# Kernel optimization log

Hardware: AMD Instinct MI355X
Metric: run time of the kernel (lower is better)

Reference implementation:

```python
import jax, jax.numpy as jnp
import numpy as np

B, N, D = 32, 512, 1024
H, DH = 8, 64
INNER = H * DH          # 512
PROJ = 512
MID = (D + PROJ) // 2   # 768
EPS = 1e-5


def _ln(x, gamma):
    # F.layer_norm over last dim, beta is a zeros buffer
    m = jnp.mean(x, axis=-1, keepdims=True)
    v = jnp.var(x, axis=-1, keepdims=True)
    return (x - m) * jax.lax.rsqrt(v + EPS) * gamma


def setup_inputs() -> dict:
    key = jax.random.key(0)
    ks = jax.random.split(key, 12)
    s = 0.02
    return {
        "x": jax.random.normal(ks[0], (B, N, D), dtype=jnp.float32),
        "pos_encoding": jax.random.normal(ks[1], (1, N, D), dtype=jnp.float32),
        "queries": jax.random.normal(ks[2], (N, D), dtype=jnp.float32),
        "ln_q_g": jnp.ones((D,), dtype=jnp.float32),
        "ln_ctx_g": jnp.ones((D,), dtype=jnp.float32),
        "Wq": jax.random.normal(ks[3], (D, INNER), dtype=jnp.float32) * s,
        "Wkv": jax.random.normal(ks[4], (D, 2 * DH), dtype=jnp.float32) * s,
        "Wout": jax.random.normal(ks[5], (INNER, D), dtype=jnp.float32) * s,
        "ln_post_g": jnp.ones((D,), dtype=jnp.float32),
        "W1": jax.random.normal(ks[6], (D, MID), dtype=jnp.float32) * s,
        "b1": jnp.zeros((MID,), dtype=jnp.float32),
        "W2": jax.random.normal(ks[7], (MID, PROJ), dtype=jnp.float32) * s,
        "b2": jnp.zeros((PROJ,), dtype=jnp.float32),
        "zero_masks": jnp.ones((B, N), dtype=jnp.int32),  # unused (masking commented out in source)
    }


def reference(x, pos_encoding, queries, ln_q_g, ln_ctx_g, Wq, Wkv, Wout,
              ln_post_g, W1, b1, W2, b2, zero_masks):
    scale = DH ** -0.5
    x = x.astype(jnp.float32) + pos_encoding                   # [B,N,D]
    q_in = jnp.broadcast_to(queries[None], (B, N, D))          # learned queries per batch

    # CrossAttention (norm_context=True, parallel_ff=False)
    qn = _ln(q_in, ln_q_g)
    ctx = _ln(x, ln_ctx_g)
    q = (qn @ Wq).reshape(B, N, H, DH).transpose(0, 2, 1, 3) * scale   # [B,H,N,DH]
    kv = ctx @ Wkv                                                     # [B,N,2*DH]
    k, v = kv[..., :DH], kv[..., DH:]                                  # shared across heads (MQA)
    sim = jnp.einsum('bhid,bjd->bhij', q, k)                           # [B,H,N,N]
    attn = jax.nn.softmax(sim, axis=-1)                                # max-subtract stable
    out = jnp.einsum('bhij,bjd->bhid', attn, v)                        # [B,H,N,DH]
    out = out.transpose(0, 2, 1, 3).reshape(B, N, INNER) @ Wout        # [B,N,D]

    out = _ln(out, ln_post_g)
    emb = jnp.mean(out, axis=1)                                        # [B,D] video embedding
    pred = jax.nn.gelu(emb @ W1 + b1, approximate=False) @ W2 + b2     # [B,PROJ]
    return pred
```

## Files before the change

kernel.cpp:

```cpp
#include <hip/hip_runtime.h>
#include <cmath>

#define Bz 32
#define Nz 512
#define Dz 1024
#define Hz 8
#define DHz 64
#define INNERz 512
#define PROJz 512
#define MIDz 768
#define EPSz 1e-5f

typedef unsigned short u16;
typedef unsigned int u32;
typedef __attribute__((ext_vector_type(8))) short short8v;
typedef __attribute__((ext_vector_type(8))) unsigned short ushort8v;
typedef __attribute__((ext_vector_type(4))) unsigned short ushort4v;
typedef __attribute__((ext_vector_type(4))) float f32x4;

__device__ __forceinline__ u16 f2bf(float x) {
  unsigned u = __float_as_uint(x);
  unsigned r = u + 0x7fff + ((u >> 16) & 1);
  return (u16)(r >> 16);
}
__device__ __forceinline__ float bf2f(u16 u) {
  return __uint_as_float(((unsigned)u) << 16);
}
__device__ __forceinline__ float fexp2(float x) {
  float r;
  asm("v_exp_f32 %0, %1" : "=v"(r) : "v"(x));
  return r;
}
__device__ __forceinline__ u32 cvtpk(float lo, float hi) {
  u32 r;
  asm("v_cvt_pk_bf16_f32 %0, %1, %2" : "=v"(r) : "v"(lo), "v"(hi));
  return r;
}

__global__ __launch_bounds__(256) void k_prepw(
    const float* __restrict__ Wkv, const float* __restrict__ Wq,
    const float* __restrict__ g_ctx, const float* __restrict__ g_q,
    u16* __restrict__ WkvTg, u16* __restrict__ WqTg,
    float* __restrict__ cskv4, float* __restrict__ csq4,
    const float* __restrict__ Wout, u16* __restrict__ WoutT) {
  __shared__ float part[64][4];
  __shared__ float sm[32][33];
  const int t = threadIdx.x;
  const int blk = blockIdx.x;
  if (blk >= 40) {
    const int bid2 = blk - 40;
    const int n0 = (bid2 & 31) * 32, k0 = (bid2 >> 5) * 32;
    {
      const int kk = t >> 3, nn = (t & 7) * 4;
      const float4 v = *reinterpret_cast<const float4*>(Wout + (size_t)(k0 + kk) * Dz + n0 + nn);
      sm[kk][nn] = v.x; sm[kk][nn + 1] = v.y; sm[kk][nn + 2] = v.z; sm[kk][nn + 3] = v.w;
    }
    __syncthreads();
    const int nn = t >> 3, kk = (t & 7) * 4;
    ushort4v pk;
#pragma unroll
    for (int j = 0; j < 4; ++j) pk[j] = f2bf(sm[kk + j][nn]);
    *reinterpret_cast<ushort4v*>(WoutT + (size_t)(n0 + nn) * INNERz + k0 + kk) = pk;
    return;
  }
  const int jg = blk >> 2, quarter = blk & 3;
  const bool isq = jg >= 2;
  const int jbase = isq ? (jg - 2) * 64 : jg * 64;
  const int j = jbase + (t & 63);
  const int dsub = t >> 6;
  const float* W = isq ? Wq : Wkv;
  const int ld = isq ? 512 : 128;
  const float* g = isq ? g_q : g_ctx;
  const float scale = isq ? 0.125f * 1.4426950408889634f : 1.f;
  u16* WT = isq ? WqTg : WkvTg;
  float partial = 0.f;
  const int d0beg = quarter * 256 + dsub * 64;
  for (int d0 = d0beg; d0 < d0beg + 64; d0 += 2) {
    const float v0 = scale * g[d0] * W[(size_t)d0 * ld + j];
    const float v1 = scale * g[d0 + 1] * W[(size_t)(d0 + 1) * ld + j];
    partial += v0 + v1;
    *(u32*)(WT + (size_t)j * Dz + d0) = (u32)f2bf(v0) | ((u32)f2bf(v1) << 16);
  }
  part[t & 63][dsub] = partial;
  __syncthreads();
  if (t < 64)
    (isq ? csq4 : cskv4)[(jbase + t) * 4 + quarter] =
        part[t][0] + part[t][1] + part[t][2] + part[t][3];
}

#define LOADB2(dst, kk)                                                        \
  {                                                                            \
    _Pragma("unroll") for (int u_ = 0; u_ < 4; ++u_)                           \
    _Pragma("unroll") for (int cf_ = 0; cf_ < 2; ++cf_)                        \
        dst[u_][cf_] =                                                         \
            *(const short8v*)(Bp + (size_t)cf_ * 16 * Dz + (kk) + u_ * 32);    \
  }

__global__ __launch_bounds__(256) void k_qproj(
    const float* __restrict__ queries, const u16* __restrict__ WT,
    const float* __restrict__ cs4, u16* __restrict__ qbuf) {
  __shared__ u16 hbuf[16 * 1024];
  __shared__ float mm[16], rr[16];
  char* hb = (char*)hbuf;
  const int t = threadIdx.x;
  const int w = t >> 6, l = t & 63;
  const int lr = l & 15, lk = l >> 4;
  const int c0 = blockIdx.y * 128 + w * 32;
  const u16* Bp = WT + (size_t)(c0 + lr) * Dz + lk * 8;
  short8v bcur[4][2], bnxt[4][2];
  LOADB2(bcur, 0);
  {
    const int r = t >> 4, c16 = t & 15;
    const long grow = (long)blockIdx.x * 16 + r;
    const float* xr = queries + grow * Dz;
    float s = 0.f, ss = 0.f;
    const int swz = (r & 7) << 4;
#pragma unroll
    for (int i = 0; i < 16; ++i) {
      const int col = c16 * 4 + i * 64;
      const float4 v = *(const float4*)(xr + col);
      s += (v.x + v.y) + (v.z + v.w);
      ss += (v.x * v.x + v.y * v.y) + (v.z * v.z + v.w * v.w);
      uint2 pk;
      pk.x = (u32)f2bf(v.x) | ((u32)f2bf(v.y) << 16);
      pk.y = (u32)f2bf(v.z) | ((u32)f2bf(v.w) << 16);
      *(uint2*)(hb + ((r * 2048 + col * 2) ^ swz)) = pk;
    }
#pragma unroll
    for (int off = 1; off <= 8; off <<= 1) { s += __shfl_xor(s, off); ss += __shfl_xor(ss, off); }
    const float mean = s * (1.f / Dz);
    const float rstd = rsqrtf(ss * (1.f / Dz) - mean * mean + EPSz);
    if (c16 == 0) { mm[r] = mean; rr[r] = rstd; }
  }
  __syncthreads();
  f32x4 acc[2];
  acc[0] = {0.f, 0.f, 0.f, 0.f};
  acc[1] = {0.f, 0.f, 0.f, 0.f};
  const int aswz = (lr & 7) << 4;
#pragma unroll
  for (int k0 = 0; k0 < Dz; k0 += 128) {
    if (k0 + 128 < Dz) LOADB2(bnxt, k0 + 128);
#pragma unroll
    for (int u = 0; u < 4; ++u) {
      const int kk = (k0 + u * 32 + lk * 8) * 2;
      const short8v a = *(const short8v*)(hb + ((lr * 2048 + kk) ^ aswz));
      acc[0] = __builtin_amdgcn_mfma_f32_16x16x32_bf16(a, bcur[u][0], acc[0], 0, 0, 0);
      acc[1] = __builtin_amdgcn_mfma_f32_16x16x32_bf16(a, bcur[u][1], acc[1], 0, 0, 0);
    }
    if (k0 + 128 < Dz) {
#pragma unroll
      for (int u = 0; u < 4; ++u) {
        bcur[u][0] = bnxt[u][0];
        bcur[u][1] = bnxt[u][1];
      }
    }
  }
  const long base = (long)blockIdx.x * 16;
#pragma unroll
  for (int cf = 0; cf < 2; ++cf) {
    const int col = c0 + cf * 16 + lr;
    const float c = cs4[col * 4] + cs4[col * 4 + 1] + cs4[col * 4 + 2] + cs4[col * 4 + 3];
#pragma unroll
    for (int q = 0; q < 4; ++q) {
      const int row = lk * 4 + q;
      qbuf[(size_t)(base + row) * INNERz + col] = f2bf(rr[row] * (acc[cf][q] - mm[row] * c));
    }
  }
}

__global__ __launch_bounds__(256) void k_ctxkv(
    const float* __restrict__ x, const float* __restrict__ pos,
    const u16* __restrict__ WT, const float* __restrict__ cs4,
    u16* __restrict__ kb, u16* __restrict__ vT) {
  __shared__ u16 hbuf[32 * 1024];
  __shared__ float mm[32], rrs[32];
  char* hb = (char*)hbuf;
  const int t = threadIdx.x;
  const int w = t >> 6, l = t & 63;
  const int lr = l & 15, lk = l >> 4;
  const int c0 = w * 32;
  const u16* Bp = WT + (size_t)(c0 + lr) * Dz + lk * 8;
  short8v bcur[4][2], bnxt[4][2];
  LOADB2(bcur, 0);
  {
    const int r2 = t >> 4, c16 = t & 15;
#pragma unroll
    for (int half = 0; half < 2; ++half) {
      const int r = r2 + half * 16;
      const long grow = (long)blockIdx.x * 32 + r;
      const int n = (int)(grow & (Nz - 1));
      const float* xr = x + grow * Dz;
      const float* pr = pos + (size_t)n * Dz;
      float s = 0.f, ss = 0.f;
      const int swz = (r & 7) << 4;
#pragma unroll
      for (int i = 0; i < 16; ++i) {
        const int col = c16 * 4 + i * 64;
        float4 v = *(const float4*)(xr + col);
        const float4 p = *(const float4*)(pr + col);
        v.x += p.x; v.y += p.y; v.z += p.z; v.w += p.w;
        s += (v.x + v.y) + (v.z + v.w);
        ss += (v.x * v.x + v.y * v.y) + (v.z * v.z + v.w * v.w);
        uint2 pk;
        pk.x = (u32)f2bf(v.x) | ((u32)f2bf(v.y) << 16);
        pk.y = (u32)f2bf(v.z) | ((u32)f2bf(v.w) << 16);
        *(uint2*)(hb + ((r * 2048 + col * 2) ^ swz)) = pk;
      }
#pragma unroll
      for (int off = 1; off <= 8; off <<= 1) { s += __shfl_xor(s, off); ss += __shfl_xor(ss, off); }
      const float mean = s * (1.f / Dz);
      const float rstd = rsqrtf(ss * (1.f / Dz) - mean * mean + EPSz);
      if (c16 == 0) { mm[r] = mean; rrs[r] = rstd; }
    }
  }
  __syncthreads();
  f32x4 acc[2][2];
#pragma unroll
  for (int rf = 0; rf < 2; ++rf)
#pragma unroll
    for (int cf = 0; cf < 2; ++cf) acc[rf][cf] = {0.f, 0.f, 0.f, 0.f};
  const int aswz = (lr & 7) << 4;
#pragma unroll
  for (int k0 = 0; k0 < Dz; k0 += 128) {
    if (k0 + 128 < Dz) LOADB2(bnxt, k0 + 128);
#pragma unroll
    for (int u = 0; u < 4; ++u) {
      const int kk = (k0 + u * 32 + lk * 8) * 2;
      const short8v a0 = *(const short8v*)(hb + ((lr * 2048 + kk) ^ aswz));
      const short8v a1 = *(const short8v*)(hb + (((lr + 16) * 2048 + kk) ^ aswz));
      acc[0][0] = __builtin_amdgcn_mfma_f32_16x16x32_bf16(a0, bcur[u][0], acc[0][0], 0, 0, 0);
      acc[0][1] = __builtin_amdgcn_mfma_f32_16x16x32_bf16(a0, bcur[u][1], acc[0][1], 0, 0, 0);
      acc[1][0] = __builtin_amdgcn_mfma_f32_16x16x32_bf16(a1, bcur[u][0], acc[1][0], 0, 0, 0);
      acc[1][1] = __builtin_amdgcn_mfma_f32_16x16x32_bf16(a1, bcur[u][1], acc[1][1], 0, 0, 0);
    }
    if (k0 + 128 < Dz) {
#pragma unroll
      for (int u = 0; u < 4; ++u) {
        bcur[u][0] = bnxt[u][0];
        bcur[u][1] = bnxt[u][1];
      }
    }
  }
  const long base = (long)blockIdx.x * 32;
  const int bb = (int)(base >> 9), nb0 = (int)(base & (Nz - 1));
#pragma unroll
  for (int rf = 0; rf < 2; ++rf)
#pragma unroll
    for (int cf = 0; cf < 2; ++cf) {
      const int col = c0 + cf * 16 + lr;
      const float c = cs4[col * 4] + cs4[col * 4 + 1] + cs4[col * 4 + 2] + cs4[col * 4 + 3];
      if (col < 64) {
#pragma unroll
        for (int q = 0; q < 4; ++q) {
          const int row = rf * 16 + lk * 4 + q;
          kb[(size_t)(base + row) * DHz + col] = f2bf(rrs[row] * (acc[rf][cf][q] - mm[row] * c));
        }
      } else {
        ushort4v pk;
#pragma unroll
        for (int q = 0; q < 4; ++q) {
          const int row = rf * 16 + lk * 4 + q;
          pk[q] = f2bf(rrs[row] * (acc[rf][cf][q] - mm[row] * c));
        }
        *(ushort4v*)(vT + ((size_t)bb * DHz + (col - 64)) * Nz + nb0 + rf * 16 + lk * 4) = pk;
      }
    }
}

__global__ __launch_bounds__(256) void k_attn(
    const u16* __restrict__ qb, const u16* __restrict__ kb,
    const u16* __restrict__ vT, u16* __restrict__ ao) {
  __shared__ u16 Ks[2][4096];
  __shared__ u16 Vs[2][4096];
  __shared__ u16 plds[4][2048];
  const int t = threadIdx.x;
  const int w = t >> 6, l = t & 63;
  const int lr = l & 15, lk = l >> 4;
  const int m0 = blockIdx.x * 64 + w * 16;
  const int h0 = blockIdx.y * 2;
  const int b = blockIdx.z;
  const u16* qr = qb + (size_t)(m0 + lr) * INNERz + h0 * DHz + lk * 8;
  const short8v aq00 = *(const short8v*)qr;
  const short8v aq01 = *(const short8v*)(qr + 32);
  const short8v aq10 = *(const short8v*)(qr + 64);
  const short8v aq11 = *(const short8v*)(qr + 96);
  const u16* kbB = kb + (size_t)b * Nz * DHz;
  const u16* vTB = vT + (size_t)b * DHz * Nz;
  char* pw0 = (char*)&plds[w][0];
  char* pw1 = (char*)&plds[w][1024];
  const int swz = (lr & 7) << 4;

  const int srow = w * 16 + (l >> 3);
  const int schunk = (l & 7) ^ (l >> 3);

#define STAGE(bufi, j0v)                                                              \
  {                                                                                   \
    _Pragma("unroll") for (int c = 0; c < 2; ++c) {                                   \
      __builtin_amdgcn_global_load_lds(                                               \
          (const __attribute__((address_space(1))) u32*)(const void*)(                \
              kbB + (size_t)((j0v) + srow + c * 8) * DHz + schunk * 8),               \
          (__attribute__((address_space(3))) u32*)(void*)(&Ks[bufi][0] + w * 1024 + c * 512), \
          16, 0, 0);                                                                  \
      __builtin_amdgcn_global_load_lds(                                               \
          (const __attribute__((address_space(1))) u32*)(const void*)(                \
              vTB + (size_t)(srow + c * 8) * Nz + (j0v) + schunk * 8),                \
          (__attribute__((address_space(3))) u32*)(void*)(&Vs[bufi][0] + w * 1024 + c * 512), \
          16, 0, 0);                                                                  \
    }                                                                                 \
  }

  f32x4 oacc0[4], oacc1[4];
#pragma unroll
  for (int dn = 0; dn < 4; ++dn) { oacc0[dn] = {0.f, 0.f, 0.f, 0.f}; oacc1[dn] = {0.f, 0.f, 0.f, 0.f}; }
  float lsum0 = 0.f, lsum1 = 0.f;

  int buf = 0;
  STAGE(0, 0);
  asm volatile("s_waitcnt vmcnt(0)" ::: "memory");
  __builtin_amdgcn_s_barrier();
  asm volatile("" ::: "memory");

  for (int tt = 0; tt < 8; ++tt) {
    if (tt < 7) STAGE(buf ^ 1, (tt + 1) * 64);
    asm volatile("" ::: "memory");
    const char* Kb = (const char*)&Ks[buf][0];
    const char* Vb = (const char*)&Vs[buf][0];
    {
      f32x4 sfr[4];
#pragma unroll
      for (int jn = 0; jn < 4; ++jn) {
        const int rbase = jn * 2048 + lr * 128;
        const short8v bk0 = *(const short8v*)(Kb + rbase + ((lk * 16) ^ swz));
        const short8v bk1 = *(const short8v*)(Kb + rbase + ((64 + lk * 16) ^ swz));
        f32x4 c = {0.f, 0.f, 0.f, 0.f};
        c = __builtin_amdgcn_mfma_f32_16x16x32_bf16(bk0, aq00, c, 0, 0, 0);
        c = __builtin_amdgcn_mfma_f32_16x16x32_bf16(bk1, aq01, c, 0, 0, 0);
        sfr[jn] = c;
      }
      float ps = 0.f;
#pragma unroll
      for (int jn = 0; jn < 4; ++jn) {
        const float e0 = fexp2(sfr[jn][0]);
        const float e1 = fexp2(sfr[jn][1]);
        const float e2 = fexp2(sfr[jn][2]);
        const float e3 = fexp2(sfr[jn][3]);
        ps += (e0 + e1) + (e2 + e3);
        const int pbase = (lr * 128 + jn * 32 + lk * 8) ^ swz;
        *(u32*)(pw0 + pbase) = cvtpk(e0, e1);
        *(u32*)(pw0 + pbase + 4) = cvtpk(e2, e3);
      }
      lsum0 += ps;
    }
    {
      f32x4 sfr[4];
#pragma unroll
      for (int jn = 0; jn < 4; ++jn) {
        const int rbase = jn * 2048 + lr * 128;
        const short8v bk0 = *(const short8v*)(Kb + rbase + ((lk * 16) ^ swz));
        const short8v bk1 = *(const short8v*)(Kb + rbase + ((64 + lk * 16) ^ swz));
        f32x4 c = {0.f, 0.f, 0.f, 0.f};
        c = __builtin_amdgcn_mfma_f32_16x16x32_bf16(bk0, aq10, c, 0, 0, 0);
        c = __builtin_amdgcn_mfma_f32_16x16x32_bf16(bk1, aq11, c, 0, 0, 0);
        sfr[jn] = c;
      }
      float ps = 0.f;
#pragma unroll
      for (int jn = 0; jn < 4; ++jn) {
        const float e0 = fexp2(sfr[jn][0]);
        const float e1 = fexp2(sfr[jn][1]);
        const float e2 = fexp2(sfr[jn][2]);
        const float e3 = fexp2(sfr[jn][3]);
        ps += (e0 + e1) + (e2 + e3);
        const int pbase = (lr * 128 + jn * 32 + lk * 8) ^ swz;
        *(u32*)(pw1 + pbase) = cvtpk(e0, e1);
        *(u32*)(pw1 + pbase + 4) = cvtpk(e2, e3);
      }
      lsum1 += ps;
    }
    const short8v pa00 = *(const short8v*)(pw0 + ((lr * 128 + lk * 16) ^ swz));
    const short8v pa01 = *(const short8v*)(pw0 + ((lr * 128 + 64 + lk * 16) ^ swz));
    const short8v pa10 = *(const short8v*)(pw1 + ((lr * 128 + lk * 16) ^ swz));
    const short8v pa11 = *(const short8v*)(pw1 + ((lr * 128 + 64 + lk * 16) ^ swz));
#pragma unroll
    for (int dn = 0; dn < 4; ++dn) {
      const int rbase = dn * 2048 + lr * 128;
      const short8v bv0 = *(const short8v*)(Vb + rbase + ((lk * 16) ^ swz));
      const short8v bv1 = *(const short8v*)(Vb + rbase + ((64 + lk * 16) ^ swz));
      f32x4 o0 = oacc0[dn];
      o0 = __builtin_amdgcn_mfma_f32_16x16x32_bf16(pa00, bv0, o0, 0, 0, 0);
      o0 = __builtin_amdgcn_mfma_f32_16x16x32_bf16(pa01, bv1, o0, 0, 0, 0);
      oacc0[dn] = o0;
      f32x4 o1 = oacc1[dn];
      o1 = __builtin_amdgcn_mfma_f32_16x16x32_bf16(pa10, bv0, o1, 0, 0, 0);
      o1 = __builtin_amdgcn_mfma_f32_16x16x32_bf16(pa11, bv1, o1, 0, 0, 0);
      oacc1[dn] = o1;
    }
    asm volatile("" ::: "memory");
    if (tt < 7) asm volatile("s_waitcnt vmcnt(0)" ::: "memory");
    __builtin_amdgcn_s_barrier();
    asm volatile("" ::: "memory");
    buf ^= 1;
  }
#undef STAGE
  lsum0 += __shfl_xor(lsum0, 16);
  lsum0 += __shfl_xor(lsum0, 32);
  lsum1 += __shfl_xor(lsum1, 16);
  lsum1 += __shfl_xor(lsum1, 32);
  float rinv0[4], rinv1[4];
#pragma unroll
  for (int r = 0; r < 4; ++r) {
    rinv0[r] = 1.f / __shfl(lsum0, lk * 4 + r, 64);
    rinv1[r] = 1.f / __shfl(lsum1, lk * 4 + r, 64);
  }
#pragma unroll
  for (int dn = 0; dn < 4; ++dn)
#pragma unroll
    for (int r = 0; r < 4; ++r) {
      const int row = m0 + lk * 4 + r;
      const size_t rbase = ((size_t)b * Nz + row) * INNERz;
      ao[rbase + h0 * DHz + dn * 16 + lr] = f2bf(oacc0[dn][r] * rinv0[r]);
      ao[rbase + (h0 + 1) * DHz + dn * 16 + lr] = f2bf(oacc1[dn][r] * rinv1[r]);
    }
}

__global__ __launch_bounds__(256) void k_wgemm(
    const u16* __restrict__ A, const u16* __restrict__ BT, u16* __restrict__ C) {
  __shared__ u16 As[128 * 64];
  __shared__ u16 Bs[128 * 64];
  const int t = threadIdx.x;
  const int w = t >> 6, l = t & 63;
  const int lin = blockIdx.y * gridDim.x + blockIdx.x;
  const int swzl = (lin & 7) * 128 + (lin >> 3);
  const int m0 = (swzl >> 3) * 128, n0 = (swzl & 7) * 128;
  const int wr = w >> 1, wc = w & 1;
  const int lr = l & 15, lk = l >> 4;

  f32x4 acc[4][4];
#pragma unroll
  for (int mt = 0; mt < 4; ++mt)
#pragma unroll
    for (int nt = 0; nt < 4; ++nt) acc[mt][nt] = {0.f, 0.f, 0.f, 0.f};

  for (int k0 = 0; k0 < INNERz; k0 += 64) {
#pragma unroll
    for (int c = 0; c < 4; ++c) {
      const int rowblk = w * 32 + c * 8;
      const int row = rowblk + (l >> 3);
      const int kb16 = (l & 7) * 8;
      __builtin_amdgcn_global_load_lds(
          (const __attribute__((address_space(1))) unsigned int*)(const void*)(
              A + (size_t)(m0 + row) * INNERz + k0 + kb16),
          (__attribute__((address_space(3))) unsigned int*)(void*)(As + rowblk * 64),
          16, 0, 0);
      __builtin_amdgcn_global_load_lds(
          (const __attribute__((address_space(1))) unsigned int*)(const void*)(
              BT + (size_t)(n0 + row) * INNERz + k0 + kb16),
          (__attribute__((address_space(3))) unsigned int*)(void*)(Bs + rowblk * 64),
          16, 0, 0);
    }
    __syncthreads();
#pragma unroll
    for (int ks = 0; ks < 2; ++ks) {
      short8v af[4], bf[4];
#pragma unroll
      for (int mt = 0; mt < 4; ++mt)
        af[mt] = *reinterpret_cast<const short8v*>(As + (wr * 64 + mt * 16 + lr) * 64 + ks * 32 + lk * 8);
#pragma unroll
      for (int nt = 0; nt < 4; ++nt)
        bf[nt] = *reinterpret_cast<const short8v*>(Bs + (wc * 64 + nt * 16 + lr) * 64 + ks * 32 + lk * 8);
#pragma unroll
      for (int mt = 0; mt < 4; ++mt)
#pragma unroll
        for (int nt = 0; nt < 4; ++nt)
          acc[mt][nt] = __builtin_amdgcn_mfma_f32_16x16x32_bf16(af[mt], bf[nt], acc[mt][nt], 0, 0, 0);
    }
    __syncthreads();
  }
#pragma unroll
  for (int mt = 0; mt < 4; ++mt)
#pragma unroll
    for (int nt = 0; nt < 4; ++nt) {
      const f32x4 a = acc[mt][nt];
#pragma unroll
      for (int r = 0; r < 4; ++r) {
        const size_t row = (size_t)m0 + wr * 64 + mt * 16 + lk * 4 + r;
        C[row * Dz + n0 + wc * 64 + nt * 16 + lr] = f2bf(a[r]);
      }
    }
}

__global__ __launch_bounds__(256) void k_lnmean(
    const u16* __restrict__ out1, float* __restrict__ pbuf) {
  const int t = threadIdx.x;
  const int w = t >> 6, l = t & 63;
  const long row0 = (long)blockIdx.x * 64 + w * 16;
  float acc[16];
#pragma unroll
  for (int j = 0; j < 16; ++j) acc[j] = 0.f;
  for (int rr = 0; rr < 16; ++rr) {
    const u16* rowp = out1 + (size_t)(row0 + rr) * Dz + l * 16;
    const ushort8v u0 = *(const ushort8v*)(rowp);
    const ushort8v u1 = *(const ushort8v*)(rowp + 8);
    float v[16];
#pragma unroll
    for (int j = 0; j < 8; ++j) { v[j] = bf2f(u0[j]); v[8 + j] = bf2f(u1[j]); }
    float s = 0.f, q = 0.f;
#pragma unroll
    for (int j = 0; j < 16; ++j) { s += v[j]; q += v[j] * v[j]; }
#pragma unroll
    for (int off = 1; off <= 32; off <<= 1) { s += __shfl_xor(s, off); q += __shfl_xor(q, off); }
    const float mean = s * (1.f / Dz);
    const float rstd = rsqrtf(q * (1.f / Dz) - mean * mean + EPSz);
#pragma unroll
    for (int j = 0; j < 16; ++j) acc[j] += (v[j] - mean) * rstd;
  }
  float* dst = pbuf + ((size_t)blockIdx.x * 4 + w) * Dz + l * 16;
#pragma unroll
  for (int j = 0; j < 4; ++j)
    *(float4*)(dst + j * 4) =
        make_float4(acc[j * 4], acc[j * 4 + 1], acc[j * 4 + 2], acc[j * 4 + 3]);
}

__global__ __launch_bounds__(256) void k_embred(
    const float* __restrict__ pbuf, const float* __restrict__ g,
    float* __restrict__ emb) {
  const int b = blockIdx.x, t = threadIdx.x;
  const float invN = 1.f / (float)Nz;
  const float* src = pbuf + (size_t)b * 32 * Dz + t * 4;
  float4 s = {0.f, 0.f, 0.f, 0.f};
#pragma unroll 8
  for (int sub = 0; sub < 32; ++sub) {
    const float4 v = *(const float4*)(src + (size_t)sub * Dz);
    s.x += v.x; s.y += v.y; s.z += v.z; s.w += v.w;
  }
  const float4 gv = *(const float4*)(g + t * 4);
  float4 o;
  o.x = s.x * gv.x * invN;
  o.y = s.y * gv.y * invN;
  o.z = s.z * gv.z * invN;
  o.w = s.w * gv.w * invN;
  *(float4*)(emb + (size_t)b * Dz + t * 4) = o;
}

__global__ __launch_bounds__(256) void k_mlp1(
    const float* __restrict__ emb, const float* __restrict__ W1,
    const float* __restrict__ b1, float* __restrict__ mid) {
  __shared__ float e[Dz];
  __shared__ float red[4][64];
  const int b = blockIdx.y, t = threadIdx.x;
  const int col0 = blockIdx.x * 64;
  *reinterpret_cast<float4*>(&e[t * 4]) =
      *reinterpret_cast<const float4*>(emb + (size_t)b * Dz + t * 4);
  __syncthreads();
  const int q = t >> 6, j = t & 63;
  float acc = 0.f;
  const float* W = W1 + (size_t)(q * 256) * MIDz + col0 + j;
#pragma unroll 8
  for (int k = 0; k < 256; ++k) acc += e[q * 256 + k] * W[(size_t)k * MIDz];
  red[q][j] = acc;
  __syncthreads();
  if (t < 64) {
    const float s = red[0][t] + red[1][t] + red[2][t] + red[3][t] + b1[col0 + t];
    mid[(size_t)b * MIDz + col0 + t] = 0.5f * s * (1.f + erff(s * 0.7071067811865475f));
  }
}

__global__ __launch_bounds__(256) void k_mlp2(
    const float* __restrict__ mid, const float* __restrict__ W2,
    const float* __restrict__ b2, float* __restrict__ out) {
  __shared__ float e[MIDz];
  __shared__ float red[4][64];
  const int b = blockIdx.y, t = threadIdx.x;
  const int col0 = blockIdx.x * 64;
  if (t < MIDz / 4)
    *reinterpret_cast<float4*>(&e[t * 4]) =
        *reinterpret_cast<const float4*>(mid + (size_t)b * MIDz + t * 4);
  __syncthreads();
  const int q = t >> 6, j = t & 63;
  float acc = 0.f;
  const float* W = W2 + (size_t)(q * 192) * PROJz + col0 + j;
#pragma unroll 8
  for (int k = 0; k < 192; ++k) acc += e[q * 192 + k] * W[(size_t)k * PROJz];
  red[q][j] = acc;
  __syncthreads();
  if (t < 64)
    out[(size_t)b * PROJz + col0 + t] =
        red[0][t] + red[1][t] + red[2][t] + red[3][t] + b2[col0 + t];
}

extern "C" void kernel_launch(void* const* d_in, const int* in_sizes, int n_in,
                              void* d_out, int out_size, void* d_ws, size_t ws_size,
                              hipStream_t stream) {
  const float* x         = (const float*)d_in[0];
  const float* pos       = (const float*)d_in[1];
  const float* queries   = (const float*)d_in[2];
  const float* ln_q_g    = (const float*)d_in[3];
  const float* ln_ctx_g  = (const float*)d_in[4];
  const float* Wq        = (const float*)d_in[5];
  const float* Wkv       = (const float*)d_in[6];
  const float* Wout      = (const float*)d_in[7];
  const float* ln_post_g = (const float*)d_in[8];
  const float* W1        = (const float*)d_in[9];
  const float* b1        = (const float*)d_in[10];
  const float* W2        = (const float*)d_in[11];
  const float* b2        = (const float*)d_in[12];
  float* out = (float*)d_out;

  char* wsb = (char*)d_ws;
  float* emb   = (float*)wsb;
  float* mid   = (float*)(wsb + 131072);
  u16*   WoutT = (u16*)(wsb + 229376);
  u16*   aobf  = (u16*)(wsb + 1277952);
  float* pbuf  = (float*)(wsb + 1277952);
  u16*   out1  = (u16*)(wsb + 18055168);
  u16*   WkvTg = (u16*)(wsb + 18055168);
  u16*   WqTg  = (u16*)(wsb + 18317312);
  float* cskv4 = (float*)(wsb + 19365888);
  float* csq4  = (float*)(wsb + 19367936);
  u16*   qbbf  = (u16*)(wsb + 19376128);
  u16*   kbbf  = (u16*)(wsb + 19900416);
  u16*   vTbf  = (u16*)(wsb + 21997568);

  k_prepw<<<552, 256, 0, stream>>>(Wkv, Wq, ln_ctx_g, ln_q_g, WkvTg, WqTg, cskv4, csq4,
                                   Wout, WoutT);
  k_qproj<<<dim3(Nz / 16, 4), 256, 0, stream>>>(queries, WqTg, csq4, qbbf);
  k_ctxkv<<<(Bz * Nz) / 32, 256, 0, stream>>>(x, pos, WkvTg, cskv4, kbbf, vTbf);
  k_attn<<<dim3(Nz / 64, Hz / 2, Bz), 256, 0, stream>>>(qbbf, kbbf, vTbf, aobf);
  k_wgemm<<<dim3(Dz / 128, (Bz * Nz) / 128), 256, 0, stream>>>(aobf, WoutT, out1);
  k_lnmean<<<(Bz * Nz) / 64, 256, 0, stream>>>(out1, pbuf);
  k_embred<<<Bz, 256, 0, stream>>>(pbuf, ln_post_g, emb);
  k_mlp1<<<dim3(MIDz / 64, Bz), 256, 0, stream>>>(emb, W1, b1, mid);
  k_mlp2<<<dim3(PROJz / 64, Bz), 256, 0, stream>>>(mid, W2, b2, out);
}
```

Baseline: 157.5 us.

## Restructure context KV projection into per-wave streaming 16-row tiles

The context LayerNorm+KV projection kernel used to stage a full 32x1024 bf16 tile in shared memory, block on a barrier, and split the 128 output columns across waves. Now each wave owns 16 rows and all 128 columns. It streams x+pos in 128-column chunks into a small private LDS buffer, feeding MFMAs chunk by chunk with no block-wide sync, and computes the row stats alongside. This cuts LDS footprint and barrier stalls so more blocks fit per CU and loads can overlap compute. In exchange, B operands now come straight from global/L2 with no register prefetch, and each wave rereads the full weight.

```diff
diff --git a/kernel.cpp b/kernel.cpp
--- a/kernel.cpp
+++ b/kernel.cpp
@@ -16,6 +16,7 @@
 typedef __attribute__((ext_vector_type(8))) short short8v;
 typedef __attribute__((ext_vector_type(8))) unsigned short ushort8v;
 typedef __attribute__((ext_vector_type(4))) unsigned short ushort4v;
+typedef __attribute__((ext_vector_type(4))) unsigned int uint4v;
 typedef __attribute__((ext_vector_type(4))) float f32x4;
 
 __device__ __forceinline__ u16 f2bf(float x) {
@@ -172,99 +173,90 @@
     const float* __restrict__ x, const float* __restrict__ pos,
     const u16* __restrict__ WT, const float* __restrict__ cs4,
     u16* __restrict__ kb, u16* __restrict__ vT) {
-  __shared__ u16 hbuf[32 * 1024];
-  __shared__ float mm[32], rrs[32];
-  char* hb = (char*)hbuf;
+  __shared__ u16 hbuf[4][16 * 128];
   const int t = threadIdx.x;
   const int w = t >> 6, l = t & 63;
   const int lr = l & 15, lk = l >> 4;
-  const int c0 = w * 32;
-  const u16* Bp = WT + (size_t)(c0 + lr) * Dz + lk * 8;
-  short8v bcur[4][2], bnxt[4][2];
-  LOADB2(bcur, 0);
-  {
-    const int r2 = t >> 4, c16 = t & 15;
-#pragma unroll
-    for (int half = 0; half < 2; ++half) {
-      const int r = r2 + half * 16;
-      const long grow = (long)blockIdx.x * 32 + r;
-      const int n = (int)(grow & (Nz - 1));
-      const float* xr = x + grow * Dz;
-      const float* pr = pos + (size_t)n * Dz;
-      float s = 0.f, ss = 0.f;
-      const int swz = (r & 7) << 4;
-#pragma unroll
-      for (int i = 0; i < 16; ++i) {
-        const int col = c16 * 4 + i * 64;
-        float4 v = *(const float4*)(xr + col);
-        const float4 p = *(const float4*)(pr + col);
+  char* hb = (char*)&hbuf[w][0];
+  const long rowbase = (long)blockIdx.x * 64 + w * 16;
+  const int n0 = (int)(rowbase & (Nz - 1));
+  const float* xr = x + (rowbase + lr) * Dz;
+  const float* pr = pos + (size_t)(n0 + lr) * Dz;
+  const int swz = (lr & 7) << 4;
+
+  f32x4 acc[8];
+#pragma unroll
+  for (int cf = 0; cf < 8; ++cf) acc[cf] = {0.f, 0.f, 0.f, 0.f};
+  float s = 0.f, ss = 0.f;
+
+  for (int chunk = 0; chunk < 8; ++chunk) {
+    const int kc = chunk * 128;
+    float4 xv[8], pv[8];
+#pragma unroll
+    for (int j = 0; j < 8; ++j) {
+      const int col = kc + lk * 32 + j * 4;
+      xv[j] = *(const float4*)(xr + col);
+      pv[j] = *(const float4*)(pr + col);
+    }
+#pragma unroll
+    for (int i = 0; i < 4; ++i) {
+      uint4v pk;
+#pragma unroll
+      for (int hh = 0; hh < 2; ++hh) {
+        float4 v = xv[i * 2 + hh];
+        const float4 p = pv[i * 2 + hh];
         v.x += p.x; v.y += p.y; v.z += p.z; v.w += p.w;
         s += (v.x + v.y) + (v.z + v.w);
         ss += (v.x * v.x + v.y * v.y) + (v.z * v.z + v.w * v.w);
-        uint2 pk;
-        pk.x = (u32)f2bf(v.x) | ((u32)f2bf(v.y) << 16);
-        pk.y = (u32)f2bf(v.z) | ((u32)f2bf(v.w) << 16);
-        *(uint2*)(hb + ((r * 2048 + col * 2) ^ swz)) = pk;
-      }
-#pragma unroll
-      for (int off = 1; off <= 8; off <<= 1) { s += __shfl_xor(s, off); ss += __shfl_xor(ss, off); }
-      const float mean = s * (1.f / Dz);
-      const float rstd = rsqrtf(ss * (1.f / Dz) - mean * mean + EPSz);
-      if (c16 == 0) { mm[r] = mean; rrs[r] = rstd; }
-    }
-  }
-  __syncthreads();
-  f32x4 acc[2][2];
-#pragma unroll
-  for (int rf = 0; rf < 2; ++rf)
-#pragma unroll
-    for (int cf = 0; cf < 2; ++cf) acc[rf][cf] = {0.f, 0.f, 0.f, 0.f};
-  const int aswz = (lr & 7) << 4;
-#pragma unroll
-  for (int k0 = 0; k0 < Dz; k0 += 128) {
-    if (k0 + 128 < Dz) LOADB2(bnxt, k0 + 128);
+        pk[hh * 2] = cvtpk(v.x, v.y);
+        pk[hh * 2 + 1] = cvtpk(v.z, v.w);
+      }
+      *(uint4v*)(hb + ((lr * 256 + lk * 64 + i * 16) ^ swz)) = pk;
+    }
+    asm volatile("s_waitcnt lgkmcnt(0)" ::: "memory");
+    __builtin_amdgcn_sched_barrier(0);
 #pragma unroll
     for (int u = 0; u < 4; ++u) {
-      const int kk = (k0 + u * 32 + lk * 8) * 2;
-      const short8v a0 = *(const short8v*)(hb + ((lr * 2048 + kk) ^ aswz));
-      const short8v a1 = *(const short8v*)(hb + (((lr + 16) * 2048 + kk) ^ aswz));
-      acc[0][0] = __builtin_amdgcn_mfma_f32_16x16x32_bf16(a0, bcur[u][0], acc[0][0], 0, 0, 0);
-      acc[0][1] = __builtin_amdgcn_mfma_f32_16x16x32_bf16(a0, bcur[u][1], acc[0][1], 0, 0, 0);
-      acc[1][0] = __builtin_amdgcn_mfma_f32_16x16x32_bf16(a1, bcur[u][0], acc[1][0], 0, 0, 0);
-      acc[1][1] = __builtin_amdgcn_mfma_f32_16x16x32_bf16(a1, bcur[u][1], acc[1][1], 0, 0, 0);
-    }
-    if (k0 + 128 < Dz) {
-#pragma unroll
-      for (int u = 0; u < 4; ++u) {
-        bcur[u][0] = bnxt[u][0];
-        bcur[u][1] = bnxt[u][1];
-      }
-    }
-  }
-  const long base = (long)blockIdx.x * 32;
-  const int bb = (int)(base >> 9), nb0 = (int)(base & (Nz - 1));
-#pragma unroll
-  for (int rf = 0; rf < 2; ++rf)
-#pragma unroll
-    for (int cf = 0; cf < 2; ++cf) {
-      const int col = c0 + cf * 16 + lr;
-      const float c = cs4[col * 4] + cs4[col * 4 + 1] + cs4[col * 4 + 2] + cs4[col * 4 + 3];
-      if (col < 64) {
-#pragma unroll
-        for (int q = 0; q < 4; ++q) {
-          const int row = rf * 16 + lk * 4 + q;
-          kb[(size_t)(base + row) * DHz + col] = f2bf(rrs[row] * (acc[rf][cf][q] - mm[row] * c));
-        }
-      } else {
-        ushort4v pk;
-#pragma unroll
-        for (int q = 0; q < 4; ++q) {
-          const int row = rf * 16 + lk * 4 + q;
-          pk[q] = f2bf(rrs[row] * (acc[rf][cf][q] - mm[row] * c));
-        }
-        *(ushort4v*)(vT + ((size_t)bb * DHz + (col - 64)) * Nz + nb0 + rf * 16 + lk * 4) = pk;
-      }
-    }
+      const short8v a = *(const short8v*)(hb + ((lr * 256 + u * 64 + lk * 16) ^ swz));
+#pragma unroll
+      for (int cf = 0; cf < 8; ++cf) {
+        const short8v bv =
+            *(const short8v*)(WT + (size_t)(cf * 16 + lr) * Dz + kc + u * 32 + lk * 8);
+        acc[cf] = __builtin_amdgcn_mfma_f32_16x16x32_bf16(a, bv, acc[cf], 0, 0, 0);
+      }
+    }
+    asm volatile("" ::: "memory");
+  }
+  s += __shfl_xor(s, 16);
+  s += __shfl_xor(s, 32);
+  ss += __shfl_xor(ss, 16);
+  ss += __shfl_xor(ss, 32);
+  const float mean_l = s * (1.f / Dz);
+  const float rstd_l = rsqrtf(ss * (1.f / Dz) - mean_l * mean_l + EPSz);
+  float mnq[4], rsq[4];
+#pragma unroll
+  for (int q = 0; q < 4; ++q) {
+    mnq[q] = __shfl(mean_l, lk * 4 + q, 64);
+    rsq[q] = __shfl(rstd_l, lk * 4 + q, 64);
+  }
+  const int bb = (int)(rowbase >> 9);
+#pragma unroll
+  for (int cf = 0; cf < 8; ++cf) {
+    const int col = cf * 16 + lr;
+    const float c = cs4[col * 4] + cs4[col * 4 + 1] + cs4[col * 4 + 2] + cs4[col * 4 + 3];
+    if (col < 64) {
+#pragma unroll
+      for (int q = 0; q < 4; ++q) {
+        const long row = rowbase + lk * 4 + q;
+        kb[(size_t)row * DHz + col] = f2bf(rsq[q] * (acc[cf][q] - mnq[q] * c));
+      }
+    } else {
+      ushort4v pk;
+#pragma unroll
+      for (int q = 0; q < 4; ++q) pk[q] = f2bf(rsq[q] * (acc[cf][q] - mnq[q] * c));
+      *(ushort4v*)(vT + ((size_t)bb * DHz + (col - 64)) * Nz + n0 + lk * 4) = pk;
+    }
+  }
 }
 
 __global__ __launch_bounds__(256) void k_attn(
@@ -624,7 +616,7 @@
   k_prepw<<<552, 256, 0, stream>>>(Wkv, Wq, ln_ctx_g, ln_q_g, WkvTg, WqTg, cskv4, csq4,
                                    Wout, WoutT);
   k_qproj<<<dim3(Nz / 16, 4), 256, 0, stream>>>(queries, WqTg, csq4, qbbf);
-  k_ctxkv<<<(Bz * Nz) / 32, 256, 0, stream>>>(x, pos, WkvTg, cskv4, kbbf, vTbf);
+  k_ctxkv<<<(Bz * Nz) / 64, 256, 0, stream>>>(x, pos, WkvTg, cskv4, kbbf, vTbf);
   k_attn<<<dim3(Nz / 64, Hz / 2, Bz), 256, 0, stream>>>(qbbf, kbbf, vTbf, aobf);
   k_wgemm<<<dim3(Dz / 128, (Bz * Nz) / 128), 256, 0, stream>>>(aobf, WoutT, out1);
   k_lnmean<<<(Bz * Nz) / 64, 256, 0, stream>>>(out1, pbuf);
```

After: 178.1 us. 13.1% more time.
